# Performance work log

Hardware: AMD Instinct MI355X
Metric: run time of the kernel (lower is better)

Reference implementation:

```python
import jax, jax.numpy as jnp
import numpy as np

B, S, H = 2, 2048, 768
NH, HD = 12, 64  # num heads, head dim


def setup_inputs() -> dict:
    key = jax.random.key(0)
    ks = jax.random.split(key, 9)
    std = 0.02
    def dense(k):
        return jax.random.normal(k, (H, H), dtype=jnp.float32) * std
    return {
        "hidden_states": jax.random.normal(ks[0], (B, S, H), dtype=jnp.float32),
        "attention_mask": jnp.ones((B, S), dtype=jnp.int32),
        "Wq": dense(ks[1]), "bq": jnp.zeros((H,), jnp.float32),
        "Wk": dense(ks[2]), "bk": jnp.zeros((H,), jnp.float32),
        "Wv": dense(ks[3]), "bv": jnp.zeros((H,), jnp.float32),
        "Wo": dense(ks[4]), "bo": jnp.zeros((H,), jnp.float32),
    }


def reference(hidden_states, attention_mask, Wq, bq, Wk, bk, Wv, bv, Wo, bo):
    # QKV projections -> [B, NH, S, HD]
    def split_heads(x):
        return x.reshape(B, S, NH, HD).transpose(0, 2, 1, 3)
    q = split_heads(hidden_states @ Wq + bq)
    k = split_heads(hidden_states @ Wk + bk)
    v = split_heads(hidden_states @ Wv + bv)
    # scaled dot-product scores [B, NH, S, S]
    scores = jnp.einsum('bhqd,bhkd->bhqk', q, k) / jnp.sqrt(jnp.float32(HD))
    adder = (1.0 - attention_mask.astype(jnp.float32)) * -10000.0
    scores = scores + adder[:, None, None, :]
    probs = jax.nn.softmax(scores, axis=-1)
    # dropout is identity at inference
    ctx = jnp.einsum('bhqk,bhkd->bhqd', probs, v)
    ctx = ctx.transpose(0, 2, 1, 3).reshape(B, S, H)
    return ctx @ Wo + bo
```

## Files before the change

kernel.cpp:

```cpp
#include <hip/hip_runtime.h>
#include <hip/hip_bf16.h>

#define DI __device__ __forceinline__

using bf16x8 = __attribute__((ext_vector_type(8))) short;
using f32x4  = __attribute__((ext_vector_type(4))) float;
using u16    = unsigned short;
using u16x4  = __attribute__((ext_vector_type(4))) unsigned short;

constexpr int Bc = 2, Sc = 2048, Hc = 768, NHc = 12, HDc = 64;
constexpr int Mc = Bc * Sc;
constexpr float L2E = 1.4426950408889634f;

DI u16 f2bf(float f) {
  union { float f; unsigned u; } c; c.f = f;
  unsigned u = c.u;
  return (u16)((u + 0x7fffu + ((u >> 16) & 1u)) >> 16);
}

DI void gload_lds16(const void* g, void* l) {
  __builtin_amdgcn_global_load_lds(
      (__attribute__((address_space(1))) void*)(g),
      (__attribute__((address_space(3))) void*)(l), 16, 0, 0);
}


__global__ void cvt_bf16(const float* __restrict__ x, u16* __restrict__ y, int n4) {
  int i = blockIdx.x * 256 + threadIdx.x;
  if (i >= n4) return;
  float4 v = reinterpret_cast<const float4*>(x)[i];
  u16x4 o;
  o[0] = f2bf(v.x); o[1] = f2bf(v.y); o[2] = f2bf(v.z); o[3] = f2bf(v.w);
  reinterpret_cast<u16x4*>(y)[i] = o;
}

__global__ void wtrans(const float* __restrict__ Wq, const float* __restrict__ Wk,
                       const float* __restrict__ Wv, const float* __restrict__ Wo,
                       u16* __restrict__ Tq, u16* __restrict__ Tk,
                       u16* __restrict__ Tv, u16* __restrict__ To) {
  __shared__ float tile[32][33];
  const float* W; u16* T;
  switch (blockIdx.z) {
    case 0:  W = Wq; T = Tq; break;
    case 1:  W = Wk; T = Tk; break;
    case 2:  W = Wv; T = Tv; break;
    default: W = Wo; T = To; break;
  }
  int tx = threadIdx.x, ty = threadIdx.y;
  int n0 = blockIdx.x * 32, k0 = blockIdx.y * 32;
#pragma unroll
  for (int j = 0; j < 4; ++j) tile[ty + j * 8][tx] = W[(k0 + ty + j * 8) * Hc + n0 + tx];
  __syncthreads();
#pragma unroll
  for (int j = 0; j < 4; ++j) T[(n0 + ty + j * 8) * Hc + k0 + tx] = f2bf(tile[tx][ty + j * 8]);
}


DI void gemm_core(const u16* __restrict__ Ag, const u16* __restrict__ Btg,
                  u16* Asm, u16* Bsm, int m0, int n0,
                  int tid, int lane, int wr, int wc, f32x4 acc[4][4]) {
  const int lo = lane & 15, hi = lane >> 4;
  const int r1 = tid >> 2, c1 = tid & 3;
  for (int kt = 0; kt < Hc / 32; ++kt) {
    const int k0 = kt * 32;
    {
      int row = r1, cg = c1 ^ ((row >> 1) & 3);
      gload_lds16(Ag  + (size_t)(row + m0) * Hc + k0 + cg * 8, Asm + tid * 8);
      gload_lds16(Btg + (size_t)(row + n0) * Hc + k0 + cg * 8, Bsm + tid * 8);
      row = r1 + 64; cg = c1 ^ ((row >> 1) & 3);
      gload_lds16(Ag  + (size_t)(row + m0) * Hc + k0 + cg * 8, Asm + (tid + 256) * 8);
      gload_lds16(Btg + (size_t)(row + n0) * Hc + k0 + cg * 8, Bsm + (tid + 256) * 8);
    }
    __syncthreads();
    bf16x8 af[4], bf[4];
#pragma unroll
    for (int m = 0; m < 4; ++m) {
      int rowa = wr * 64 + m * 16 + lo;
      af[m] = *reinterpret_cast<const bf16x8*>(Asm + rowa * 32 + ((hi ^ ((rowa >> 1) & 3)) * 8));
      int rowb = wc * 64 + m * 16 + lo;
      bf[m] = *reinterpret_cast<const bf16x8*>(Bsm + rowb * 32 + ((hi ^ ((rowb >> 1) & 3)) * 8));
    }
#pragma unroll
    for (int m = 0; m < 4; ++m)
#pragma unroll
      for (int n = 0; n < 4; ++n)
        acc[m][n] = __builtin_amdgcn_mfma_f32_16x16x32_bf16(af[m], bf[n], acc[m][n], 0, 0, 0);
    __syncthreads();
  }
}


__launch_bounds__(256)
__global__ void qkv_gemm(const u16* __restrict__ Xb,
                         const u16* __restrict__ Wtq, const u16* __restrict__ Wtk,
                         const u16* __restrict__ Wtv,
                         const float* __restrict__ bq, const float* __restrict__ bk,
                         const float* __restrict__ bv,
                         u16* __restrict__ Qo, u16* __restrict__ Ko, u16* __restrict__ Vto) {
  __shared__ __attribute__((aligned(16))) u16 Asm[128 * 32];
  __shared__ __attribute__((aligned(16))) u16 Bsm[128 * 32];
  const int tid = threadIdx.x, lane = tid & 63, w = tid >> 6;
  const int wr = w >> 1, wc = w & 1;
  const int m0 = blockIdx.x * 128, n0 = blockIdx.y * 128;
  const int z = blockIdx.z;
  const u16* Bt = (z == 0) ? Wtq : ((z == 1) ? Wtk : Wtv);
  const float* bias = (z == 0) ? bq : ((z == 1) ? bk : bv);
  f32x4 acc[4][4] = {};
  gemm_core(Xb, Bt, Asm, Bsm, m0, n0, tid, lane, wr, wc, acc);
  const int lo = lane & 15, hi = lane >> 4;
  const float scl = (z == 0) ? 0.125f : 1.0f;
#pragma unroll
  for (int m = 0; m < 4; ++m)
#pragma unroll
    for (int n = 0; n < 4; ++n)
#pragma unroll
      for (int r = 0; r < 4; ++r) {
        int gm = m0 + wr * 64 + m * 16 + hi * 4 + r;
        int gn = n0 + wc * 64 + n * 16 + lo;
        float v = (acc[m][n][r] + bias[gn]) * scl;
        int b = gm >> 11, s = gm & 2047, h = gn >> 6, d = gn & 63;
        u16 bv16 = f2bf(v);
        if (z == 2) Vto[((b * NHc + h) * HDc + d) * Sc + s] = bv16;
        else {
          int idx = (((b * NHc + h) * Sc) + s) * HDc + d;
          if (z == 0) Qo[idx] = bv16; else Ko[idx] = bv16;
        }
      }
}


__launch_bounds__(256)
__global__ void out_gemm(const u16* __restrict__ Ctx, const u16* __restrict__ Wto,
                         const float* __restrict__ bo, float* __restrict__ out) {
  __shared__ __attribute__((aligned(16))) u16 Asm[128 * 32];
  __shared__ __attribute__((aligned(16))) u16 Bsm[128 * 32];
  const int tid = threadIdx.x, lane = tid & 63, w = tid >> 6;
  const int wr = w >> 1, wc = w & 1;
  const int m0 = blockIdx.x * 128, n0 = blockIdx.y * 128;
  f32x4 acc[4][4] = {};
  gemm_core(Ctx, Wto, Asm, Bsm, m0, n0, tid, lane, wr, wc, acc);
  const int lo = lane & 15, hi = lane >> 4;
#pragma unroll
  for (int m = 0; m < 4; ++m)
#pragma unroll
    for (int n = 0; n < 4; ++n)
#pragma unroll
      for (int r = 0; r < 4; ++r) {
        int gm = m0 + wr * 64 + m * 16 + hi * 4 + r;
        int gn = n0 + wc * 64 + n * 16 + lo;
        out[(size_t)gm * Hc + gn] = acc[m][n][r] + bo[gn];
      }
}


__launch_bounds__(256)
__global__ void attn(const u16* __restrict__ Qg, const u16* __restrict__ Kg,
                     const u16* __restrict__ Vtg, const int* __restrict__ maskg,
                     u16* __restrict__ ctxg) {
  __shared__ __attribute__((aligned(16))) u16 Ksm[64 * 64];
  __shared__ __attribute__((aligned(16))) u16 Vsm[64 * 64];
  __shared__ __attribute__((aligned(16))) u16 Psm[4][16 * 64];
  const int tid = threadIdx.x, lane = tid & 63, w = tid >> 6;
  const int lo = lane & 15, hi = lane >> 4;
  const int q0 = blockIdx.x * 64;
  const int bh = blockIdx.y;
  const int b = bh / NHc, h = bh % NHc;
  const u16* Qh = Qg + (size_t)bh * Sc * HDc;
  const u16* Kh = Kg + (size_t)bh * Sc * HDc;
  const u16* Vh = Vtg + (size_t)bh * HDc * Sc;
  const int* maskb = maskg + b * Sc;

  const int qrow = q0 + w * 16 + lo;
  bf16x8 qf[2];
  qf[0] = *reinterpret_cast<const bf16x8*>(Qh + (size_t)qrow * HDc + hi * 8);
  qf[1] = *reinterpret_cast<const bf16x8*>(Qh + (size_t)qrow * HDc + 32 + hi * 8);

  f32x4 oacc[4] = {};
  float mrow[4] = {-1e30f, -1e30f, -1e30f, -1e30f};
  float lrow[4] = {0.f, 0.f, 0.f, 0.f};

  const int ch1 = tid, row1 = ch1 >> 3, cs1 = ch1 & 7, cg1 = cs1 ^ (row1 & 7);
  const int ch2 = tid + 256, row2 = ch2 >> 3, cs2 = ch2 & 7, cg2 = cs2 ^ (row2 & 7);

  for (int kv0 = 0; kv0 < Sc; kv0 += 64) {
    gload_lds16(Kh + (size_t)(kv0 + row1) * HDc + cg1 * 8, Ksm + ch1 * 8);
    gload_lds16(Kh + (size_t)(kv0 + row2) * HDc + cg2 * 8, Ksm + ch2 * 8);
    gload_lds16(Vh + (size_t)row1 * Sc + kv0 + cg1 * 8, Vsm + ch1 * 8);
    gload_lds16(Vh + (size_t)row2 * Sc + kv0 + cg2 * 8, Vsm + ch2 * 8);
    __syncthreads();

    f32x4 sacc[4] = {};
#pragma unroll
    for (int n = 0; n < 4; ++n) {
#pragma unroll
      for (int ks = 0; ks < 2; ++ks) {
        int row = n * 16 + lo;
        bf16x8 kf = *reinterpret_cast<const bf16x8*>(
            Ksm + row * 64 + (((ks * 4 + hi) ^ (row & 7)) * 8));
        sacc[n] = __builtin_amdgcn_mfma_f32_16x16x32_bf16(qf[ks], kf, sacc[n], 0, 0, 0);
      }
      int kp = kv0 + n * 16 + lo;
      float add = (1.0f - (float)maskb[kp]) * -10000.0f;
#pragma unroll
      for (int r = 0; r < 4; ++r) sacc[n][r] += add;
    }

    float tmax[4];
#pragma unroll
    for (int r = 0; r < 4; ++r)
      tmax[r] = fmaxf(fmaxf(sacc[0][r], sacc[1][r]), fmaxf(sacc[2][r], sacc[3][r]));
#pragma unroll
    for (int off = 1; off < 16; off <<= 1)
#pragma unroll
      for (int r = 0; r < 4; ++r) tmax[r] = fmaxf(tmax[r], __shfl_xor(tmax[r], off, 64));

    float scale[4], psum[4];
#pragma unroll
    for (int r = 0; r < 4; ++r) {
      float mnew = fmaxf(mrow[r], tmax[r]);
      scale[r] = exp2f((mrow[r] - mnew) * L2E);
      mrow[r] = mnew;
      psum[r] = 0.f;
    }
#pragma unroll
    for (int n = 0; n < 4; ++n)
#pragma unroll
      for (int r = 0; r < 4; ++r) {
        float p = exp2f((sacc[n][r] - mrow[r]) * L2E);
        sacc[n][r] = p;
        psum[r] += p;
      }
#pragma unroll
    for (int off = 1; off < 16; off <<= 1)
#pragma unroll
      for (int r = 0; r < 4; ++r) psum[r] += __shfl_xor(psum[r], off, 64);
#pragma unroll
    for (int r = 0; r < 4; ++r) lrow[r] = lrow[r] * scale[r] + psum[r];
#pragma unroll
    for (int n = 0; n < 4; ++n)
#pragma unroll
      for (int r = 0; r < 4; ++r) oacc[n][r] *= scale[r];

    u16* Pw = &Psm[w][0];
#pragma unroll
    for (int n = 0; n < 4; ++n)
#pragma unroll
      for (int r = 0; r < 4; ++r) {
        int prow = hi * 4 + r, pcol = n * 16 + lo;
        Pw[prow * 64 + (pcol ^ ((prow & 7) << 3))] = f2bf(sacc[n][r]);
      }
#pragma unroll
    for (int n = 0; n < 4; ++n) {
#pragma unroll
      for (int ks = 0; ks < 2; ++ks) {
        bf16x8 pf = *reinterpret_cast<const bf16x8*>(
            Pw + lo * 64 + ((ks * 32 + hi * 8) ^ ((lo & 7) << 3)));
        int vrow = n * 16 + lo;
        bf16x8 vf = *reinterpret_cast<const bf16x8*>(
            Vsm + vrow * 64 + (((ks * 4 + hi) ^ (vrow & 7)) * 8));
        oacc[n] = __builtin_amdgcn_mfma_f32_16x16x32_bf16(pf, vf, oacc[n], 0, 0, 0);
      }
    }
    __syncthreads();
  }

#pragma unroll
  for (int r = 0; r < 4; ++r) {
    float inv = 1.0f / lrow[r];
#pragma unroll
    for (int n = 0; n < 4; ++n) {
      int gq = q0 + w * 16 + hi * 4 + r;
      int gd = n * 16 + lo;
      ctxg[(size_t)(b * Sc + gq) * Hc + h * HDc + gd] = f2bf(oacc[n][r] * inv);
    }
  }
}


extern "C" void kernel_launch(void* const* d_in, const int* in_sizes, int n_in,
                              void* d_out, int out_size, void* d_ws, size_t ws_size,
                              hipStream_t stream) {
  const float* hs  = (const float*)d_in[0];
  const int* mask  = (const int*)d_in[1];
  const float* Wq  = (const float*)d_in[2];
  const float* bq  = (const float*)d_in[3];
  const float* Wk  = (const float*)d_in[4];
  const float* bk  = (const float*)d_in[5];
  const float* Wv  = (const float*)d_in[6];
  const float* bv  = (const float*)d_in[7];
  const float* Wo  = (const float*)d_in[8];
  const float* bo  = (const float*)d_in[9];

  char* ws = (char*)d_ws;
  u16* Xb  = (u16*)(ws);
  u16* Wtq = (u16*)(ws + 6291456);
  u16* Wtk = Wtq + 589824;
  u16* Wtv = Wtk + 589824;
  u16* Wto = Wtv + 589824;
  u16* Qb  = (u16*)(ws + 11010048);
  u16* Kb  = Qb + 3145728;
  u16* Vtb = Kb + 3145728;
  u16* Ctx = Vtb + 3145728;

  cvt_bf16<<<(Mc * Hc / 4 + 255) / 256, 256, 0, stream>>>(hs, Xb, Mc * Hc / 4);
  wtrans<<<dim3(24, 24, 4), dim3(32, 8), 0, stream>>>(Wq, Wk, Wv, Wo, Wtq, Wtk, Wtv, Wto);
  qkv_gemm<<<dim3(32, 6, 3), 256, 0, stream>>>(Xb, Wtq, Wtk, Wtv, bq, bk, bv, Qb, Kb, Vtb);
  attn<<<dim3(Sc / 64, Bc * NHc), 256, 0, stream>>>(Qb, Kb, Vtb, mask, Ctx);
  out_gemm<<<dim3(32, 6), 256, 0, stream>>>(Ctx, Wto, bo, (float*)d_out);
}
```

Before: 160.1 us.

## Double-buffer attention K/V tiles, fold log2e into Q, compute row sums via MFMA

The attention kernel now double-buffers K/V tiles in LDS so the next tile's async global-to-LDS loads overlap compute, using explicit vmcnt waits and raw barriers. The log2(e) factor moves into the Q scale and into a mask-adder table precomputed in LDS, which removes per-element multiplies and global mask reads. Row sums come from an MFMA against a ones vector instead of shuffle reductions, and blocks are remapped so each XCD handles a contiguous set of heads for L2 locality. It also uses paired bf16 conversion. The cost is more LDS (double buffers plus an 8KB adder table) and added synchronisation complexity.

```diff
diff --git a/kernel.cpp b/kernel.cpp
--- a/kernel.cpp
+++ b/kernel.cpp
@@ -16,6 +16,13 @@
   union { float f; unsigned u; } c; c.f = f;
   unsigned u = c.u;
   return (u16)((u + 0x7fffu + ((u >> 16) & 1u)) >> 16);
+}
+
+DI unsigned f2bf2(float a, float b) {
+  float2 t; t.x = a; t.y = b;
+  __hip_bfloat162 h = __float22bfloat162_rn(t);
+  union { __hip_bfloat162 h; unsigned u; } c; c.h = h;
+  return c.u;
 }
 
 DI void gload_lds16(const void* g, void* l) {
@@ -108,7 +115,7 @@
   f32x4 acc[4][4] = {};
   gemm_core(Xb, Bt, Asm, Bsm, m0, n0, tid, lane, wr, wc, acc);
   const int lo = lane & 15, hi = lane >> 4;
-  const float scl = (z == 0) ? 0.125f : 1.0f;
+  const float scl = (z == 0) ? 0.125f * L2E : 1.0f;
 #pragma unroll
   for (int m = 0; m < 4; ++m)
 #pragma unroll
@@ -157,37 +164,79 @@
 __global__ void attn(const u16* __restrict__ Qg, const u16* __restrict__ Kg,
                      const u16* __restrict__ Vtg, const int* __restrict__ maskg,
                      u16* __restrict__ ctxg) {
-  __shared__ __attribute__((aligned(16))) u16 Ksm[64 * 64];
-  __shared__ __attribute__((aligned(16))) u16 Vsm[64 * 64];
+  __shared__ __attribute__((aligned(16))) u16 Ksm[2][64 * 64];
+  __shared__ __attribute__((aligned(16))) u16 Vsm[2][64 * 64];
   __shared__ __attribute__((aligned(16))) u16 Psm[4][16 * 64];
+  __shared__ __attribute__((aligned(16))) float Adm[Sc];
+
   const int tid = threadIdx.x, lane = tid & 63, w = tid >> 6;
   const int lo = lane & 15, hi = lane >> 4;
-  const int q0 = blockIdx.x * 64;
-  const int bh = blockIdx.y;
-  const int b = bh / NHc, h = bh % NHc;
-  const u16* Qh = Qg + (size_t)bh * Sc * HDc;
-  const u16* Kh = Kg + (size_t)bh * Sc * HDc;
-  const u16* Vh = Vtg + (size_t)bh * HDc * Sc;
+
+  const int id = blockIdx.x;
+  const int xcd = id & 7, sub = id >> 3;
+  const int head = xcd * 3 + (sub >> 5);
+  const int q0 = (sub & 31) * 64;
+  const int b = head / NHc, h = head % NHc;
+
+  const u16* Qh = Qg + (size_t)head * Sc * HDc;
+  const u16* Kh = Kg + (size_t)head * Sc * HDc;
+  const u16* Vh = Vtg + (size_t)head * HDc * Sc;
   const int* maskb = maskg + b * Sc;
+
+  for (int i = tid; i < Sc / 4; i += 256) {
+    int4 mv = reinterpret_cast<const int4*>(maskb)[i];
+    float4 a;
+    a.x = (1.0f - (float)mv.x) * (-10000.0f * L2E);
+    a.y = (1.0f - (float)mv.y) * (-10000.0f * L2E);
+    a.z = (1.0f - (float)mv.z) * (-10000.0f * L2E);
+    a.w = (1.0f - (float)mv.w) * (-10000.0f * L2E);
+    reinterpret_cast<float4*>(Adm)[i] = a;
+  }
 
   const int qrow = q0 + w * 16 + lo;
   bf16x8 qf[2];
   qf[0] = *reinterpret_cast<const bf16x8*>(Qh + (size_t)qrow * HDc + hi * 8);
   qf[1] = *reinterpret_cast<const bf16x8*>(Qh + (size_t)qrow * HDc + 32 + hi * 8);
 
+  bf16x8 onesf;
+#pragma unroll
+  for (int i = 0; i < 8; ++i) onesf[i] = (short)0x3F80;
+
   f32x4 oacc[4] = {};
+  f32x4 lacc = {};
   float mrow[4] = {-1e30f, -1e30f, -1e30f, -1e30f};
-  float lrow[4] = {0.f, 0.f, 0.f, 0.f};
-
-  const int ch1 = tid, row1 = ch1 >> 3, cs1 = ch1 & 7, cg1 = cs1 ^ (row1 & 7);
-  const int ch2 = tid + 256, row2 = ch2 >> 3, cs2 = ch2 & 7, cg2 = cs2 ^ (row2 & 7);
-
-  for (int kv0 = 0; kv0 < Sc; kv0 += 64) {
-    gload_lds16(Kh + (size_t)(kv0 + row1) * HDc + cg1 * 8, Ksm + ch1 * 8);
-    gload_lds16(Kh + (size_t)(kv0 + row2) * HDc + cg2 * 8, Ksm + ch2 * 8);
-    gload_lds16(Vh + (size_t)row1 * Sc + kv0 + cg1 * 8, Vsm + ch1 * 8);
-    gload_lds16(Vh + (size_t)row2 * Sc + kv0 + cg2 * 8, Vsm + ch2 * 8);
-    __syncthreads();
+
+  const int ch1 = tid, row1 = ch1 >> 3, cg1 = (ch1 & 7) ^ (row1 & 7);
+  const int ch2 = tid + 256, row2 = ch2 >> 3, cg2 = (ch2 & 7) ^ (row2 & 7);
+
+  __syncthreads();
+
+  gload_lds16(Kh + (size_t)row1 * HDc + cg1 * 8, &Ksm[0][0] + ch1 * 8);
+  gload_lds16(Kh + (size_t)row2 * HDc + cg2 * 8, &Ksm[0][0] + ch2 * 8);
+  gload_lds16(Vh + (size_t)row1 * Sc + cg1 * 8, &Vsm[0][0] + ch1 * 8);
+  gload_lds16(Vh + (size_t)row2 * Sc + cg2 * 8, &Vsm[0][0] + ch2 * 8);
+
+  int cur = 0;
+  constexpr int NT = Sc / 64;
+  for (int t = 0; t < NT; ++t) {
+    if (t + 1 < NT) {
+      const int kvn = (t + 1) * 64;
+      u16* Kn = &Ksm[cur ^ 1][0];
+      u16* Vn = &Vsm[cur ^ 1][0];
+      gload_lds16(Kh + (size_t)(kvn + row1) * HDc + cg1 * 8, Kn + ch1 * 8);
+      gload_lds16(Kh + (size_t)(kvn + row2) * HDc + cg2 * 8, Kn + ch2 * 8);
+      gload_lds16(Vh + (size_t)row1 * Sc + kvn + cg1 * 8, Vn + ch1 * 8);
+      gload_lds16(Vh + (size_t)row2 * Sc + kvn + cg2 * 8, Vn + ch2 * 8);
+      asm volatile("s_waitcnt vmcnt(4)" ::: "memory");
+    } else {
+      asm volatile("s_waitcnt vmcnt(0)" ::: "memory");
+    }
+    __builtin_amdgcn_sched_barrier(0);
+    __builtin_amdgcn_s_barrier();
+    __builtin_amdgcn_sched_barrier(0);
+
+    const u16* Ks = &Ksm[cur][0];
+    const u16* Vs = &Vsm[cur][0];
 
     f32x4 sacc[4] = {};
 #pragma unroll
@@ -196,11 +245,10 @@
       for (int ks = 0; ks < 2; ++ks) {
         int row = n * 16 + lo;
         bf16x8 kf = *reinterpret_cast<const bf16x8*>(
-            Ksm + row * 64 + (((ks * 4 + hi) ^ (row & 7)) * 8));
+            Ks + row * 64 + (((ks * 4 + hi) ^ (row & 7)) * 8));
         sacc[n] = __builtin_amdgcn_mfma_f32_16x16x32_bf16(qf[ks], kf, sacc[n], 0, 0, 0);
       }
-      int kp = kv0 + n * 16 + lo;
-      float add = (1.0f - (float)maskb[kp]) * -10000.0f;
+      float add = Adm[t * 64 + n * 16 + lo];
 #pragma unroll
       for (int r = 0; r < 4; ++r) sacc[n][r] += add;
     }
@@ -214,59 +262,63 @@
 #pragma unroll
       for (int r = 0; r < 4; ++r) tmax[r] = fmaxf(tmax[r], __shfl_xor(tmax[r], off, 64));
 
-    float scale[4], psum[4];
+    float scale[4];
 #pragma unroll
     for (int r = 0; r < 4; ++r) {
       float mnew = fmaxf(mrow[r], tmax[r]);
-      scale[r] = exp2f((mrow[r] - mnew) * L2E);
+      scale[r] = exp2f(mrow[r] - mnew);
       mrow[r] = mnew;
-      psum[r] = 0.f;
     }
 #pragma unroll
     for (int n = 0; n < 4; ++n)
 #pragma unroll
-      for (int r = 0; r < 4; ++r) {
-        float p = exp2f((sacc[n][r] - mrow[r]) * L2E);
-        sacc[n][r] = p;
-        psum[r] += p;
-      }
-#pragma unroll
-    for (int off = 1; off < 16; off <<= 1)
-#pragma unroll
-      for (int r = 0; r < 4; ++r) psum[r] += __shfl_xor(psum[r], off, 64);
-#pragma unroll
-    for (int r = 0; r < 4; ++r) lrow[r] = lrow[r] * scale[r] + psum[r];
+      for (int r = 0; r < 4; ++r) sacc[n][r] = exp2f(sacc[n][r] - mrow[r]);
 #pragma unroll
     for (int n = 0; n < 4; ++n)
 #pragma unroll
       for (int r = 0; r < 4; ++r) oacc[n][r] *= scale[r];
+#pragma unroll
+    for (int r = 0; r < 4; ++r) lacc[r] *= scale[r];
 
     u16* Pw = &Psm[w][0];
 #pragma unroll
-    for (int n = 0; n < 4; ++n)
-#pragma unroll
-      for (int r = 0; r < 4; ++r) {
-        int prow = hi * 4 + r, pcol = n * 16 + lo;
-        Pw[prow * 64 + (pcol ^ ((prow & 7) << 3))] = f2bf(sacc[n][r]);
-      }
-#pragma unroll
     for (int n = 0; n < 4; ++n) {
-#pragma unroll
-      for (int ks = 0; ks < 2; ++ks) {
-        bf16x8 pf = *reinterpret_cast<const bf16x8*>(
-            Pw + lo * 64 + ((ks * 32 + hi * 8) ^ ((lo & 7) << 3)));
-        int vrow = n * 16 + lo;
-        bf16x8 vf = *reinterpret_cast<const bf16x8*>(
-            Vsm + vrow * 64 + (((ks * 4 + hi) ^ (vrow & 7)) * 8));
-        oacc[n] = __builtin_amdgcn_mfma_f32_16x16x32_bf16(pf, vf, oacc[n], 0, 0, 0);
-      }
-    }
-    __syncthreads();
+      unsigned u01 = f2bf2(sacc[n][0], sacc[n][1]);
+      unsigned u23 = f2bf2(sacc[n][2], sacc[n][3]);
+      int pcol = n * 16 + lo;
+      int r0 = hi * 4;
+      Pw[(r0 + 0) * 64 + (pcol ^ (((r0 + 0) & 7) << 3))] = (u16)(u01 & 0xffff);
+      Pw[(r0 + 1) * 64 + (pcol ^ (((r0 + 1) & 7) << 3))] = (u16)(u01 >> 16);
+      Pw[(r0 + 2) * 64 + (pcol ^ (((r0 + 2) & 7) << 3))] = (u16)(u23 & 0xffff);
+      Pw[(r0 + 3) * 64 + (pcol ^ (((r0 + 3) & 7) << 3))] = (u16)(u23 >> 16);
+    }
+
+    bf16x8 pf0 = *reinterpret_cast<const bf16x8*>(
+        Pw + lo * 64 + ((hi * 8) ^ ((lo & 7) << 3)));
+    bf16x8 pf1 = *reinterpret_cast<const bf16x8*>(
+        Pw + lo * 64 + ((32 + hi * 8) ^ ((lo & 7) << 3)));
+    lacc = __builtin_amdgcn_mfma_f32_16x16x32_bf16(pf0, onesf, lacc, 0, 0, 0);
+    lacc = __builtin_amdgcn_mfma_f32_16x16x32_bf16(pf1, onesf, lacc, 0, 0, 0);
+#pragma unroll
+    for (int n = 0; n < 4; ++n) {
+      int vrow = n * 16 + lo;
+      bf16x8 vf0 = *reinterpret_cast<const bf16x8*>(
+          Vs + vrow * 64 + ((hi ^ (vrow & 7)) * 8));
+      bf16x8 vf1 = *reinterpret_cast<const bf16x8*>(
+          Vs + vrow * 64 + (((4 + hi) ^ (vrow & 7)) * 8));
+      oacc[n] = __builtin_amdgcn_mfma_f32_16x16x32_bf16(pf0, vf0, oacc[n], 0, 0, 0);
+      oacc[n] = __builtin_amdgcn_mfma_f32_16x16x32_bf16(pf1, vf1, oacc[n], 0, 0, 0);
+    }
+
+    __builtin_amdgcn_sched_barrier(0);
+    __builtin_amdgcn_s_barrier();
+    __builtin_amdgcn_sched_barrier(0);
+    cur ^= 1;
   }
 
 #pragma unroll
   for (int r = 0; r < 4; ++r) {
-    float inv = 1.0f / lrow[r];
+    float inv = 1.0f / lacc[r];
 #pragma unroll
     for (int n = 0; n < 4; ++n) {
       int gq = q0 + w * 16 + hi * 4 + r;
@@ -305,6 +357,6 @@
   cvt_bf16<<<(Mc * Hc / 4 + 255) / 256, 256, 0, stream>>>(hs, Xb, Mc * Hc / 4);
   wtrans<<<dim3(24, 24, 4), dim3(32, 8), 0, stream>>>(Wq, Wk, Wv, Wo, Wtq, Wtk, Wtv, Wto);
   qkv_gemm<<<dim3(32, 6, 3), 256, 0, stream>>>(Xb, Wtq, Wtk, Wtv, bq, bk, bv, Qb, Kb, Vtb);
-  attn<<<dim3(Sc / 64, Bc * NHc), 256, 0, stream>>>(Qb, Kb, Vtb, mask, Ctx);
+  attn<<<768, 256, 0, stream>>>(Qb, Kb, Vtb, mask, Ctx);
   out_gemm<<<dim3(32, 6), 256, 0, stream>>>(Ctx, Wto, bo, (float*)d_out);
 }
```

New measurement: 141.0 us. 1.13x faster.
